# Kernel optimization log

Hardware: AMD Instinct MI355X
Metric: run time of the kernel (lower is better)

The kernel has to match this reference:

```python
import jax, jax.numpy as jnp
from jax import lax
import numpy as np

EPS = 1e-4  # self.epsilon
UPS = 16    # 224 / 14 : adaptive_avg_pool2d upsample == nearest repeat when out % in == 0


def _conv1x1(h, W, b):
    # 1x1 conv as channel matmul: h [B,C,H,W], W [O,C]
    return jnp.einsum('bchw,oc->bohw', h, W) + b[None, :, None, None]


def _forward(x, mascaras, Wf, bf, W1, b1, W2, b2, W3, b3, W4, b4, prototypes, last_W, topk_k):
    x = x[:, 0:3, :, :]
    # stand-in backbone: conv 3->512, k16 s16 VALID, ReLU -> [B,512,14,14]
    f = lax.conv_general_dilated(x, Wf, window_strides=(16, 16), padding='VALID')
    f = jax.nn.relu(f + bf[None, :, None, None])
    # add-on bottleneck: 512->256->256->128->128, final sigmoid -> [B,128,14,14]
    h = jax.nn.relu(_conv1x1(f, W1, b1))
    h = jax.nn.relu(_conv1x1(h, W2, b2))
    h = jax.nn.relu(_conv1x1(h, W3, b3))
    h = jax.nn.sigmoid(_conv1x1(h, W4, b4))
    # _l2_convolution with 1x1 prototypes == torch.cdist between patch vectors and prototypes
    f2 = jnp.sum(h * h, axis=1)                    # [B,H,W]
    p2 = jnp.sum(prototypes * prototypes, axis=1)  # [P]
    inner = jnp.einsum('bchw,pc->bphw', h, prototypes)
    d2 = jnp.maximum(f2[:, None] + p2[None, :, None, None] - 2.0 * inner, 0.0)
    distances = jnp.sqrt(d2)                       # [B,P,H,W] (cdist = euclidean, not squared)
    B, P, H, W = distances.shape
    dflat = distances.reshape(B, P, H * W)
    # min_distances: avg of k smallest distances per prototype
    neg_top, _ = lax.top_k(-dflat, topk_k)
    min_distances = jnp.mean(-neg_top, axis=-1)    # [B,P]
    # log similarity
    act = jnp.log((distances + 1.0) / (distances + EPS))
    top_act, _ = lax.top_k(act.reshape(B, P, H * W), topk_k)
    proto_act = jnp.mean(top_act, axis=-1)         # [B,P]
    logits = proto_act @ last_W.T                  # [B,num_classes]
    # adaptive_avg_pool2d 14->224 with integer ratio == repeat by 16 in H and W
    upsampled_activation = jnp.repeat(jnp.repeat(act, UPS, axis=2), UPS, axis=3)
    return logits, min_distances, upsampled_activation


def setup_inputs() -> dict:
    key = jax.random.key(0)
    ks = jax.random.split(key, 12)
    rn = lambda k, s, sc=0.05: jax.random.normal(k, s, jnp.float32) * sc
    return {
        'x': jax.random.normal(ks[0], (16, 3, 224, 224), jnp.float32),
        'mascaras': jax.random.uniform(ks[1], (16, 1, 224, 224), jnp.float32),
        'Wf': rn(ks[2], (512, 3, 16, 16)),
        'bf': jnp.zeros((512,), jnp.float32),
        'W1': rn(ks[3], (256, 512)), 'b1': jnp.zeros((256,), jnp.float32),
        'W2': rn(ks[4], (256, 256)), 'b2': jnp.zeros((256,), jnp.float32),
        'W3': rn(ks[5], (128, 256)), 'b3': jnp.zeros((128,), jnp.float32),
        'W4': rn(ks[6], (128, 128)), 'b4': jnp.zeros((128,), jnp.float32),
        'prototypes': jax.random.uniform(ks[7], (60, 128), jnp.float32),  # torch.rand init
        'last_W': rn(ks[8], (3, 60)),
        'topk_k': 5,
    }


def reference(x, mascaras, Wf, bf, W1, b1, W2, b2, W3, b3, W4, b4, prototypes, last_W, topk_k):
    return _forward(x, mascaras, Wf, bf, W1, b1, W2, b2, W3, b3, W4, b4, prototypes, last_W, topk_k)
```

## Files before the change

### kernel.cpp

```cpp
#include <hip/hip_runtime.h>
#include <hip/hip_bf16.h>

using short8  = __attribute__((ext_vector_type(8))) short;
using ushort8 = __attribute__((ext_vector_type(8))) unsigned short;
using floatx4 = __attribute__((ext_vector_type(4))) float;

#define EPSV 1e-4f

__device__ __forceinline__ unsigned short bfbits(float f) {
  __hip_bfloat16 h = __float2bfloat16(f);
  return *reinterpret_cast<unsigned short*>(&h);
}

__global__ void cvt_weights(const float4* __restrict__ Wf, const float4* __restrict__ W1,
                            const float4* __restrict__ W2, const float4* __restrict__ W3,
                            const float4* __restrict__ W4, ushort4* __restrict__ dst) {
  int t = blockIdx.x * 256 + threadIdx.x;
  const float4* src; int off;
  if (t < 98304)       { src = Wf; off = 0; }
  else if (t < 131072) { src = W1; off = 98304; }
  else if (t < 147456) { src = W2; off = 131072; }
  else if (t < 155648) { src = W3; off = 147456; }
  else                 { src = W4; off = 155648; }
  float4 v = src[t - off];
  ushort4 o;
  o.x = bfbits(v.x); o.y = bfbits(v.y); o.z = bfbits(v.z); o.w = bfbits(v.w);
  dst[t] = o;
}

__global__ void im2col_kernel(const float* __restrict__ x,
                              __hip_bfloat16* __restrict__ A0) {
  int t = blockIdx.x * 256 + threadIdx.x;
  int kh = t & 15;
  int rest = t >> 4;
  int c = rest % 3;
  int row = rest / 3;
  int b = row / 196;
  int ij = row - b * 196;
  int i = ij / 14;
  int j = ij - i * 14;
  const float4* s4 = reinterpret_cast<const float4*>(
      x + ((size_t)(b * 3 + c) * 224 + (size_t)(i * 16 + kh)) * 224 + j * 16);
  __hip_bfloat16* dst = A0 + (size_t)row * 768 + c * 256 + kh * 16;
  float4 v0 = s4[0], v1 = s4[1], v2 = s4[2], v3 = s4[3];
  ushort8 o0, o1;
  o0[0] = bfbits(v0.x); o0[1] = bfbits(v0.y); o0[2] = bfbits(v0.z); o0[3] = bfbits(v0.w);
  o0[4] = bfbits(v1.x); o0[5] = bfbits(v1.y); o0[6] = bfbits(v1.z); o0[7] = bfbits(v1.w);
  o1[0] = bfbits(v2.x); o1[1] = bfbits(v2.y); o1[2] = bfbits(v2.z); o1[3] = bfbits(v2.w);
  o1[4] = bfbits(v3.x); o1[5] = bfbits(v3.y); o1[6] = bfbits(v3.z); o1[7] = bfbits(v3.w);
  ushort8* d8 = reinterpret_cast<ushort8*>(dst);
  d8[0] = o0;
  d8[1] = o1;
}

template <int ACT>
__global__ void gemm_bt(const __hip_bfloat16* __restrict__ A,
                        const __hip_bfloat16* __restrict__ W,
                        const float* __restrict__ bias,
                        __hip_bfloat16* __restrict__ C,
                        int M, int N, int K) {
  const int m0 = blockIdx.x * 64;
  const int n0 = blockIdx.y * 64;
  const int lane = threadIdx.x;
  const int r = lane & 15;
  const int q = lane >> 4;

  const __hip_bfloat16* Abase = A + (size_t)(m0 + r) * K + q * 8;
  const __hip_bfloat16* Wbase = W + (size_t)(n0 + r) * K + q * 8;

  floatx4 acc[4][4] = {};
  for (int k = 0; k < K; k += 32) {
    short8 a[4], b[4];
#pragma unroll
    for (int i = 0; i < 4; ++i) {
      a[i] = *reinterpret_cast<const short8*>(Abase + (size_t)i * 16 * K + k);
      b[i] = *reinterpret_cast<const short8*>(Wbase + (size_t)i * 16 * K + k);
    }
#pragma unroll
    for (int mi = 0; mi < 4; ++mi)
#pragma unroll
      for (int ni = 0; ni < 4; ++ni)
        acc[mi][ni] = __builtin_amdgcn_mfma_f32_16x16x32_bf16(a[mi], b[ni], acc[mi][ni], 0, 0, 0);
  }

#pragma unroll
  for (int mi = 0; mi < 4; ++mi) {
#pragma unroll
    for (int ni = 0; ni < 4; ++ni) {
      int col = n0 + ni * 16 + r;
      float bv = bias[col];
#pragma unroll
      for (int rr = 0; rr < 4; ++rr) {
        int row = m0 + mi * 16 + q * 4 + rr;
        float v = acc[mi][ni][rr] + bv;
        if (ACT == 0) v = fmaxf(v, 0.0f);
        else          v = 1.0f / (1.0f + __expf(-v));
        C[(size_t)row * N + col] = __float2bfloat16(v);
      }
    }
  }
}

__global__ void dist_act_kernel(const __hip_bfloat16* __restrict__ h4,
                                const float* __restrict__ proto,
                                float* __restrict__ dist,
                                float* __restrict__ act) {
  __shared__ float hs[64][129];
  __shared__ float ps[60][128];
  const int t = threadIdx.x;
  const int pos0 = blockIdx.x * 64;

  for (int i = t; i < 64 * 128; i += 256) {
    int pp = i >> 7, kk = i & 127;
    hs[pp][kk] = __bfloat162float(h4[(size_t)(pos0 + pp) * 128 + kk]);
  }
  for (int i = t; i < 60 * 128; i += 256)
    ps[i >> 7][i & 127] = proto[i];
  __syncthreads();

  for (int qq = t; qq < 64 * 60; qq += 256) {
    int p = qq >> 6;
    int pos = qq & 63;
    float s = 0.0f;
#pragma unroll 8
    for (int k = 0; k < 128; ++k) {
      float dv = hs[pos][k] - ps[p][k];
      s = fmaf(dv, dv, s);
    }
    float d = sqrtf(s);
    float a = __logf((d + 1.0f) / (d + EPSV));
    int gpos = pos0 + pos;
    int bimg = gpos / 196;
    int hw = gpos - bimg * 196;
    size_t idx = ((size_t)bimg * 60 + p) * 196 + hw;
    dist[idx] = d;
    act[idx] = a;
  }
}

__global__ void topk_kernel(const float* __restrict__ dist,
                            float* __restrict__ proto_act,
                            float* __restrict__ out_mind) {
  const int wid = threadIdx.x >> 6;
  const int lane = threadIdx.x & 63;
  const int u = blockIdx.x * 4 + wid;
  const float* rowp = dist + (size_t)u * 196;

  float v[4];
#pragma unroll
  for (int i = 0; i < 4; ++i) {
    int idx = lane + 64 * i;
    v[i] = (idx < 196) ? rowp[idx] : 1e30f;
  }

  float sd = 0.0f, sa = 0.0f;
#pragma unroll
  for (int round = 0; round < 5; ++round) {
    float lmin = fminf(fminf(v[0], v[1]), fminf(v[2], v[3]));
    float m = lmin;
#pragma unroll
    for (int off = 32; off >= 1; off >>= 1)
      m = fminf(m, __shfl_xor(m, off));
    unsigned long long msk = __ballot(lmin == m);
    int leader = __ffsll((long long)msk) - 1;
    if (lane == leader) {
      if (v[0] == m)      v[0] = 1e30f;
      else if (v[1] == m) v[1] = 1e30f;
      else if (v[2] == m) v[2] = 1e30f;
      else                v[3] = 1e30f;
    }
    sd += m;
    sa += __logf((m + 1.0f) / (m + EPSV));
  }
  if (lane == 0) {
    out_mind[u] = sd * 0.2f;
    proto_act[u] = sa * 0.2f;
  }
}

__global__ void logits_kernel(const float* __restrict__ proto_act,
                              const float* __restrict__ lastW,
                              float* __restrict__ out) {
  int t = threadIdx.x;
  if (t < 48) {
    int b = t / 3, c = t - b * 3;
    float s = 0.0f;
    for (int p = 0; p < 60; ++p)
      s += proto_act[b * 60 + p] * lastW[c * 60 + p];
    out[t] = s;
  }
}

__global__ void upsample_kernel(const float* __restrict__ act,
                                float* __restrict__ up) {
  int t = blockIdx.x * 256 + threadIdx.x;
  int col4 = t % 56;
  int rem = t / 56;
  int y = rem % 224;
  int bp = rem / 224;
  float v = act[(size_t)bp * 196 + (y >> 4) * 14 + (col4 >> 2)];
  float4 val;
  val.x = v; val.y = v; val.z = v; val.w = v;
  reinterpret_cast<float4*>(up)[t] = val;
}

extern "C" void kernel_launch(void* const* d_in, const int* in_sizes, int n_in,
                              void* d_out, int out_size, void* d_ws, size_t ws_size,
                              hipStream_t stream) {
  const float* x     = (const float*)d_in[0];
  const float* Wf    = (const float*)d_in[2];
  const float* bf    = (const float*)d_in[3];
  const float* W1    = (const float*)d_in[4];
  const float* b1    = (const float*)d_in[5];
  const float* W2    = (const float*)d_in[6];
  const float* b2    = (const float*)d_in[7];
  const float* W3    = (const float*)d_in[8];
  const float* b3    = (const float*)d_in[9];
  const float* W4    = (const float*)d_in[10];
  const float* b4    = (const float*)d_in[11];
  const float* proto = (const float*)d_in[12];
  const float* lastW = (const float*)d_in[13];

  char* ws = (char*)d_ws;
  __hip_bfloat16* WfB = (__hip_bfloat16*)(ws + 0);
  __hip_bfloat16* W1B = (__hip_bfloat16*)(ws + 786432);
  __hip_bfloat16* W2B = (__hip_bfloat16*)(ws + 1048576);
  __hip_bfloat16* W3B = (__hip_bfloat16*)(ws + 1179648);
  __hip_bfloat16* W4B = (__hip_bfloat16*)(ws + 1245184);
  __hip_bfloat16* A0 = (__hip_bfloat16*)(ws + 1310720);
  __hip_bfloat16* h1 = (__hip_bfloat16*)(ws + 1310720);
  __hip_bfloat16* h2 = (__hip_bfloat16*)(ws + 2916352);
  __hip_bfloat16* h3 = (__hip_bfloat16*)(ws + 4521984);
  __hip_bfloat16* f  = (__hip_bfloat16*)(ws + 6128128);
  __hip_bfloat16* h4 = (__hip_bfloat16*)(ws + 6128128);
  float* dist = (float*)(ws + 6930944);
  float* act  = (float*)(ws + 7683584);
  float* pact = (float*)(ws + 8436224);

  float* out        = (float*)d_out;
  float* out_logits = out;
  float* out_mind   = out + 48;
  float* out_up     = out + 1008;

  cvt_weights<<<624, 256, 0, stream>>>((const float4*)Wf, (const float4*)W1,
                                       (const float4*)W2, (const float4*)W3,
                                       (const float4*)W4, (ushort4*)WfB);
  im2col_kernel<<<588, 256, 0, stream>>>(x, A0);
  gemm_bt<0><<<dim3(49, 8), 64, 0, stream>>>(A0, WfB, bf, f,  3136, 512, 768);
  gemm_bt<0><<<dim3(49, 4), 64, 0, stream>>>(f,  W1B, b1, h1, 3136, 256, 512);
  gemm_bt<0><<<dim3(49, 4), 64, 0, stream>>>(h1, W2B, b2, h2, 3136, 256, 256);
  gemm_bt<0><<<dim3(49, 2), 64, 0, stream>>>(h2, W3B, b3, h3, 3136, 128, 256);
  gemm_bt<1><<<dim3(49, 2), 64, 0, stream>>>(h3, W4B, b4, h4, 3136, 128, 128);
  dist_act_kernel<<<49, 256, 0, stream>>>(h4, proto, dist, act);
  topk_kernel<<<240, 256, 0, stream>>>(dist, pact, out_mind);
  logits_kernel<<<1, 64, 0, stream>>>(pact, lastW, out_logits);
  upsample_kernel<<<47100, 256, 0, stream>>>(act, out_up);
}
```

Before: 334.8 us.

## Fuse bottleneck MLP layers and distance computation into one LDS-resident kernel

```diff
diff --git a/kernel.cpp b/kernel.cpp
--- a/kernel.cpp
+++ b/kernel.cpp
@@ -53,7 +53,6 @@
   d8[1] = o1;
 }
 
-template <int ACT>
 __global__ void gemm_bt(const __hip_bfloat16* __restrict__ A,
                         const __hip_bfloat16* __restrict__ W,
                         const float* __restrict__ bias,
@@ -92,39 +91,115 @@
 #pragma unroll
       for (int rr = 0; rr < 4; ++rr) {
         int row = m0 + mi * 16 + q * 4 + rr;
-        float v = acc[mi][ni][rr] + bv;
-        if (ACT == 0) v = fmaxf(v, 0.0f);
-        else          v = 1.0f / (1.0f + __expf(-v));
+        float v = fmaxf(acc[mi][ni][rr] + bv, 0.0f);
         C[(size_t)row * N + col] = __float2bfloat16(v);
       }
     }
   }
 }
 
-__global__ void dist_act_kernel(const __hip_bfloat16* __restrict__ h4,
-                                const float* __restrict__ proto,
-                                float* __restrict__ dist,
-                                float* __restrict__ act) {
-  __shared__ float hs[64][129];
-  __shared__ float ps[60][128];
+__device__ __forceinline__ short8 frag_from_lds(const float* p) {
+  float4 f0 = *reinterpret_cast<const float4*>(p);
+  float4 f1 = *reinterpret_cast<const float4*>(p + 4);
+  short8 a;
+  a[0] = bfbits(f0.x); a[1] = bfbits(f0.y); a[2] = bfbits(f0.z); a[3] = bfbits(f0.w);
+  a[4] = bfbits(f1.x); a[5] = bfbits(f1.y); a[6] = bfbits(f1.z); a[7] = bfbits(f1.w);
+  return a;
+}
+
+template <int N, int K, int ACT>
+__device__ __forceinline__ void layer_lds(const float* __restrict__ A, int astride,
+                                          const __hip_bfloat16* __restrict__ W,
+                                          const float* __restrict__ bias,
+                                          float* __restrict__ C, int cstride,
+                                          int w, int r, int q) {
+  constexpr int NA = N / 64;
+  const int n0 = w * (N / 4);
+  floatx4 acc[NA] = {};
+#pragma unroll
+  for (int k0 = 0; k0 < K; k0 += 32) {
+    short8 a = frag_from_lds(A + r * astride + k0 + q * 8);
+#pragma unroll
+    for (int ni = 0; ni < NA; ++ni) {
+      short8 b = *reinterpret_cast<const short8*>(W + (size_t)(n0 + ni * 16 + r) * K + k0 + q * 8);
+      acc[ni] = __builtin_amdgcn_mfma_f32_16x16x32_bf16(a, b, acc[ni], 0, 0, 0);
+    }
+  }
+#pragma unroll
+  for (int ni = 0; ni < NA; ++ni) {
+    float bv = bias[n0 + ni * 16 + r];
+#pragma unroll
+    for (int rr = 0; rr < 4; ++rr) {
+      float v = acc[ni][rr] + bv;
+      v = (ACT == 0) ? fmaxf(v, 0.0f) : 1.0f / (1.0f + __expf(-v));
+      C[(q * 4 + rr) * cstride + n0 + ni * 16 + r] = v;
+    }
+  }
+}
+
+__global__ __launch_bounds__(256) void mlp_dist_kernel(
+    const __hip_bfloat16* __restrict__ f,
+    const __hip_bfloat16* __restrict__ W1B, const float* __restrict__ b1,
+    const __hip_bfloat16* __restrict__ W2B, const float* __restrict__ b2,
+    const __hip_bfloat16* __restrict__ W3B, const float* __restrict__ b3,
+    const __hip_bfloat16* __restrict__ W4B, const float* __restrict__ b4,
+    const float* __restrict__ proto,
+    float* __restrict__ dist, float* __restrict__ act) {
+  __shared__ float bufA[16 * 260];
+  __shared__ float bufB[16 * 260];
+  __shared__ float ps[60 * 132];
   const int t = threadIdx.x;
-  const int pos0 = blockIdx.x * 64;
-
-  for (int i = t; i < 64 * 128; i += 256) {
-    int pp = i >> 7, kk = i & 127;
-    hs[pp][kk] = __bfloat162float(h4[(size_t)(pos0 + pp) * 128 + kk]);
-  }
-  for (int i = t; i < 60 * 128; i += 256)
-    ps[i >> 7][i & 127] = proto[i];
+  const int w = t >> 6;
+  const int lane = t & 63;
+  const int r = lane & 15;
+  const int q = lane >> 4;
+  const int pos0 = blockIdx.x * 16;
+
+  {
+    const float4* p4 = reinterpret_cast<const float4*>(proto);
+    for (int i = t; i < 1920; i += 256) {
+      int p = i >> 5, kc = i & 31;
+      *reinterpret_cast<float4*>(&ps[p * 132 + kc * 4]) = p4[i];
+    }
+  }
+
+  {
+    const __hip_bfloat16* Ab = f + (size_t)(pos0 + r) * 512 + q * 8;
+    floatx4 acc[4] = {};
+#pragma unroll
+    for (int k0 = 0; k0 < 512; k0 += 32) {
+      short8 a = *reinterpret_cast<const short8*>(Ab + k0);
+#pragma unroll
+      for (int ni = 0; ni < 4; ++ni) {
+        short8 b = *reinterpret_cast<const short8*>(W1B + (size_t)(w * 64 + ni * 16 + r) * 512 + k0 + q * 8);
+        acc[ni] = __builtin_amdgcn_mfma_f32_16x16x32_bf16(a, b, acc[ni], 0, 0, 0);
+      }
+    }
+#pragma unroll
+    for (int ni = 0; ni < 4; ++ni) {
+      float bv = b1[w * 64 + ni * 16 + r];
+#pragma unroll
+      for (int rr = 0; rr < 4; ++rr) {
+        float v = fmaxf(acc[ni][rr] + bv, 0.0f);
+        bufA[(q * 4 + rr) * 260 + w * 64 + ni * 16 + r] = v;
+      }
+    }
+  }
   __syncthreads();
-
-  for (int qq = t; qq < 64 * 60; qq += 256) {
-    int p = qq >> 6;
-    int pos = qq & 63;
+  layer_lds<256, 256, 0>(bufA, 260, W2B, b2, bufB, 260, w, r, q);
+  __syncthreads();
+  layer_lds<128, 256, 0>(bufB, 260, W3B, b3, bufA, 132, w, r, q);
+  __syncthreads();
+  layer_lds<128, 128, 1>(bufA, 132, W4B, b4, bufB, 132, w, r, q);
+  __syncthreads();
+
+  for (int qq = t; qq < 960; qq += 256) {
+    int p = qq >> 4;
+    int pos = qq & 15;
     float s = 0.0f;
 #pragma unroll 8
     for (int k = 0; k < 128; ++k) {
-      float dv = hs[pos][k] - ps[p][k];
+      float dv = bufB[pos * 132 + k] - ps[p * 132 + k];
       s = fmaf(dv, dv, s);
     }
     float d = sqrtf(s);
@@ -228,14 +303,10 @@
   __hip_bfloat16* W3B = (__hip_bfloat16*)(ws + 1179648);
   __hip_bfloat16* W4B = (__hip_bfloat16*)(ws + 1245184);
   __hip_bfloat16* A0 = (__hip_bfloat16*)(ws + 1310720);
-  __hip_bfloat16* h1 = (__hip_bfloat16*)(ws + 1310720);
-  __hip_bfloat16* h2 = (__hip_bfloat16*)(ws + 2916352);
-  __hip_bfloat16* h3 = (__hip_bfloat16*)(ws + 4521984);
   __hip_bfloat16* f  = (__hip_bfloat16*)(ws + 6128128);
-  __hip_bfloat16* h4 = (__hip_bfloat16*)(ws + 6128128);
-  float* dist = (float*)(ws + 6930944);
-  float* act  = (float*)(ws + 7683584);
-  float* pact = (float*)(ws + 8436224);
+  float* dist = (float*)(ws + 9339392);
+  float* act  = (float*)(ws + 10092032);
+  float* pact = (float*)(ws + 10844672);
 
   float* out        = (float*)d_out;
   float* out_logits = out;
@@ -246,12 +317,9 @@
                                        (const float4*)W2, (const float4*)W3,
                                        (const float4*)W4, (ushort4*)WfB);
   im2col_kernel<<<588, 256, 0, stream>>>(x, A0);
-  gemm_bt<0><<<dim3(49, 8), 64, 0, stream>>>(A0, WfB, bf, f,  3136, 512, 768);
-  gemm_bt<0><<<dim3(49, 4), 64, 0, stream>>>(f,  W1B, b1, h1, 3136, 256, 512);
-  gemm_bt<0><<<dim3(49, 4), 64, 0, stream>>>(h1, W2B, b2, h2, 3136, 256, 256);
-  gemm_bt<0><<<dim3(49, 2), 64, 0, stream>>>(h2, W3B, b3, h3, 3136, 128, 256);
-  gemm_bt<1><<<dim3(49, 2), 64, 0, stream>>>(h3, W4B, b4, h4, 3136, 128, 128);
-  dist_act_kernel<<<49, 256, 0, stream>>>(h4, proto, dist, act);
+  gemm_bt<<<dim3(49, 8), 64, 0, stream>>>(A0, WfB, bf, f, 3136, 512, 768);
+  mlp_dist_kernel<<<196, 256, 0, stream>>>(f, W1B, b1, W2B, b2, W3B, b3, W4B, b4,
+                                           proto, dist, act);
   topk_kernel<<<240, 256, 0, stream>>>(dist, pact, out_mind);
   logits_kernel<<<1, 64, 0, stream>>>(pact, lastW, out_logits);
   upsample_kernel<<<47100, 256, 0, stream>>>(act, out_up);
```

New measurement: 286.0 us. -14.6%, faster.
